# Kernel optimization log

Hardware: AMD Instinct MI355X
Metric: run time of the kernel (lower is better)

Reference implementation:

```python
import jax, jax.numpy as jnp
import numpy as np

N, E, C_IN, C_OUT, NHEADS = 100000, 1600000, 128, 128, 4


def setup_inputs() -> dict:
    key = jax.random.key(0)
    k1, k2, k3, k4 = jax.random.split(key, 4)
    x = jax.random.normal(k1, (N, C_IN), dtype=jnp.float32)
    edge_index = jax.random.randint(k2, (2, E), 0, N, dtype=jnp.int32)
    batch_slices_x = jnp.array([0, N], dtype=jnp.int32)
    # glorot-style init scale
    weight = jax.random.normal(k3, (C_IN, C_OUT), dtype=jnp.float32) * (1.0 / np.sqrt(C_IN))
    att_weight = jax.random.normal(k4, (1, NHEADS, 2 * (C_OUT // NHEADS)), dtype=jnp.float32) * 0.1
    return {"x": x, "edge_index": edge_index, "batch_slices_x": batch_slices_x,
            "weight": weight, "att_weight": att_weight}


def reference(x, edge_index, batch_slices_x, weight, att_weight):
    # Eval-mode VotePoolLayer: hard attention via per-source-node argmax (scatter_max),
    # cat head-combine, no bias, att_act = identity, then graph pruning (relabel=False).
    n = x.shape[0]
    nheads = att_weight.shape[1]
    c1h = att_weight.shape[2] // 2  # out_channels per head

    h = (x @ weight).reshape(n, nheads, c1h)  # (N, H, c)
    w_j = att_weight[0, :, :c1h]              # (H, c) weights for source (x_j)
    w_i = att_weight[0, :, c1h:]              # (H, c) weights for target (x_i)
    # alpha[e,h] = sum_c h[src[e],h,c]*w_j[h,c] + h[dst[e],h,c]*w_i[h,c]
    s_j = jnp.einsum('nhc,hc->nh', h, w_j)    # (N, H)
    s_i = jnp.einsum('nhc,hc->nh', h, w_i)    # (N, H)

    src, dst = edge_index[0], edge_index[1]
    alpha = s_j[src] + s_i[dst]               # (E, H)

    # scatter_max argmax over edges grouped by src, per head -> one-hot alpha
    e = alpha.shape[0]
    seg_max = jax.ops.segment_max(alpha, src, num_segments=n)  # (N, H)
    is_max = alpha == seg_max[src]                             # (E, H)
    eids = jnp.arange(e, dtype=jnp.int32)[:, None]             # (E, 1)
    cand = jnp.where(is_max, eids, jnp.int32(e))
    seg_argmax = jax.ops.segment_min(cand, src, num_segments=n)  # (N, H) edge ids
    alpha_1hot = (eids == seg_argmax[src]).astype(h.dtype)       # (E, H)

    # message passing: weighted source features, scatter-add at destination
    msg = h[src] * alpha_1hot[:, :, None]                        # (E, H, c)
    out = jax.ops.segment_sum(msg, dst, num_segments=n)          # (N, H, c)
    out = out.reshape(n, nheads * c1h)                           # cat combine

    # edge selection (eval branch): alpha.sum(dim=1) > 0
    edge_select = alpha_1hot.sum(axis=1) > 0                     # (E,)

    # prune (relabel=False): nodes = unique(dst[edge_select]); keep edges with both
    # endpoints in node set; zero out features of the selected nodes.
    node_mask = jnp.zeros(n, dtype=jnp.int32).at[dst].max(edge_select.astype(jnp.int32)) > 0
    edge_keep = node_mask[src] & node_mask[dst]                  # (E,) subgraph edge mask
    x_out = jnp.where(node_mask[:, None], jnp.float32(0), out)

    return x_out, edge_keep, node_mask, batch_slices_x
```

## Files before the change

kernel.cpp:

```cpp
#include <hip/hip_runtime.h>
#include <stdint.h>

typedef unsigned long long u64;
typedef unsigned int u32;
typedef unsigned short u16;
typedef u32 u32x4 __attribute__((ext_vector_type(4)));
typedef float f32x4 __attribute__((ext_vector_type(4)));

#define CIN 128
#define NN 100000
#define EE 1600000

__device__ __forceinline__ float bf2f(u16 v) {
    union { u32 u; float f; } cv;
    cv.u = ((u32)v) << 16;
    return cv.f;
}

__device__ __forceinline__ u16 f2bf(float f) {
    u32 b = __float_as_uint(f);
    return (u16)((b + 0x7FFFu + ((b >> 16) & 1u)) >> 16);
}

__device__ __forceinline__ u32 mono32(float f) {
    u32 u = __float_as_uint(f);
    return ((int)u >= 0) ? (u | 0x80000000u) : ~u;
}

__global__ __launch_bounds__(256, 4) void k_s(const u16* __restrict__ x,
                                              const u16* __restrict__ W,
                                              const u16* __restrict__ att,
                                              ushort4* __restrict__ sjb,
                                              ushort4* __restrict__ sib,
                                              u32x4* __restrict__ xout16, int n_xout16,
                                              u32x4* __restrict__ seg16, int n_seg16,
                                              int* __restrict__ nm, int n_nodes) {
    int stride = gridDim.x * blockDim.x;
    int tid = blockIdx.x * blockDim.x + threadIdx.x;
    u32x4 z = { 0, 0, 0, 0 };
    for (int i = tid; i < n_xout16; i += stride) __builtin_nontemporal_store(z, &xout16[i]);
    for (int i = tid; i < n_seg16; i += stride) __builtin_nontemporal_store(z, &seg16[i]);
    for (int i = tid; i < n_nodes; i += stride) nm[i] = 0;

    __shared__ float Vl[1024];
    for (int slot = threadIdx.x; slot < 1024; slot += 256) {
        int k = slot >> 3, h8 = slot & 7;
        int head = h8 & 3;
        int off = (h8 < 4) ? 0 : 32;
        float acc = 0.0f;
        #pragma unroll
        for (int c = 0; c < 32; ++c)
            acc += bf2f(W[k * CIN + head * 32 + c]) * bf2f(att[head * 64 + off + c]);
        Vl[slot] = acc;
    }
    __syncthreads();

    for (int n = tid; n < n_nodes; n += stride) {
        const uint4* row = (const uint4*)(x + (size_t)n * CIN);
        float acc[8];
        #pragma unroll
        for (int h = 0; h < 8; ++h) acc[h] = 0.0f;
        #pragma unroll 4
        for (int q = 0; q < 16; ++q) {
            uint4 v = row[q];
            u32 w[4] = { v.x, v.y, v.z, v.w };
            #pragma unroll
            for (int j = 0; j < 4; ++j) {
                float x0 = bf2f((u16)(w[j] & 0xFFFFu));
                float x1 = bf2f((u16)(w[j] >> 16));
                int k0 = q * 8 + j * 2;
                #pragma unroll
                for (int h = 0; h < 8; ++h) acc[h] += x0 * Vl[k0 * 8 + h];
                #pragma unroll
                for (int h = 0; h < 8; ++h) acc[h] += x1 * Vl[(k0 + 1) * 8 + h];
            }
        }
        ushort4 a, b;
        a.x = f2bf(acc[0]); a.y = f2bf(acc[1]); a.z = f2bf(acc[2]); a.w = f2bf(acc[3]);
        b.x = f2bf(acc[4]); b.y = f2bf(acc[5]); b.z = f2bf(acc[6]); b.w = f2bf(acc[7]);
        sjb[n] = a;
        sib[n] = b;
    }
}

__global__ __launch_bounds__(256) void k_edge(const int* __restrict__ ei,
                                              const ushort4* __restrict__ sjb,
                                              const ushort4* __restrict__ sib,
                                              u64* __restrict__ seg, int n_edges) {
    int e = blockIdx.x * blockDim.x + threadIdx.x;
    if (e >= n_edges) return;
    int src = ei[e], dst = ei[n_edges + e];
    ushort4 sj = sjb[src];
    ushort4 si = sib[dst];
    u64 lo = (u64)(u32)(~(u32)e);
    u64* slot = seg + (size_t)src * 4;
    ulonglong2 c01 = *(const ulonglong2*)(slot);
    ulonglong2 c23 = *(const ulonglong2*)(slot + 2);
    u64 k0 = ((u64)mono32(bf2f(sj.x) + bf2f(si.x)) << 32) | lo;
    u64 k1 = ((u64)mono32(bf2f(sj.y) + bf2f(si.y)) << 32) | lo;
    u64 k2 = ((u64)mono32(bf2f(sj.z) + bf2f(si.z)) << 32) | lo;
    u64 k3 = ((u64)mono32(bf2f(sj.w) + bf2f(si.w)) << 32) | lo;
    if (k0 > c01.x) atomicMax(&slot[0], k0);
    if (k1 > c01.y) atomicMax(&slot[1], k1);
    if (k2 > c23.x) atomicMax(&slot[2], k2);
    if (k3 > c23.y) atomicMax(&slot[3], k3);
}

__global__ void k_select(const int* __restrict__ ei, const u64* __restrict__ seg,
                         int* __restrict__ nm, int n4, int n_edges) {
    int t = blockIdx.x * blockDim.x + threadIdx.x;
    if (t >= n4) return;
    u64 m = seg[t];
    if (m) {
        int e = (int)(~(u32)m);
        nm[ei[n_edges + e]] = 1;
    }
}

__global__ void k_final(const int* __restrict__ ei, const int* __restrict__ nm,
                        const int* __restrict__ slices, float* __restrict__ out,
                        int n_edges, int n_nodes, int ek_off, int nm_off, int sl_off) {
    int t = blockIdx.x * blockDim.x + threadIdx.x;
    int e0 = 4 * t;
    if (e0 < n_edges) {
        int4 srcs = ((const int4*)ei)[t];
        int4 dsts = ((const int4*)(ei + n_edges))[t];
        f32x4 v;
        v.x = (nm[srcs.x] & nm[dsts.x]) ? 1.0f : 0.0f;
        v.y = (nm[srcs.y] & nm[dsts.y]) ? 1.0f : 0.0f;
        v.z = (nm[srcs.z] & nm[dsts.z]) ? 1.0f : 0.0f;
        v.w = (nm[srcs.w] & nm[dsts.w]) ? 1.0f : 0.0f;
        __builtin_nontemporal_store(v, &((f32x4*)(out + ek_off))[t]);
    }
    if (t < n_nodes) out[nm_off + t] = nm[t] ? 1.0f : 0.0f;
    if (t < 2) out[sl_off + t] = (float)slices[t];
}

extern "C" void kernel_launch(void* const* d_in, const int* in_sizes, int n_in,
                              void* d_out, int out_size, void* d_ws, size_t ws_size,
                              hipStream_t stream) {
    const u16* x = nullptr; const int* ei = nullptr; const int* sl = nullptr;
    const u16* W = nullptr; const u16* att = nullptr;
    for (int i = 0; i < n_in; ++i) {
        switch (in_sizes[i]) {
            case NN * CIN:   x   = (const u16*)d_in[i]; break;
            case 2 * EE:     ei  = (const int*)d_in[i]; break;
            case 2:          sl  = (const int*)d_in[i]; break;
            case CIN * CIN:  W   = (const u16*)d_in[i]; break;
            case 256:        att = (const u16*)d_in[i]; break;
            default: break;
        }
    }
    if (!x || !ei || !sl || !W || !att) return;

    float* out = (float*)d_out;
    const int N = NN;
    const int E = EE;
    const int N4 = N * 4;

    const int ek_off = N * CIN;
    const int nm_off = ek_off + E;
    const int sl_off = nm_off + N;

    char* ws = (char*)d_ws;
    ushort4* sjb = (ushort4*)(ws);
    ushort4* sib = (ushort4*)(ws + (size_t)N * 8);
    int*     nm  = (int*)    (ws + (size_t)N * 16);
    u64*     seg = (u64*)    (ws + (size_t)N * 20);

    const int n_xout16 = N * CIN / 4;
    const int n_seg16  = N4 / 2;

    k_s<<<1280, 256, 0, stream>>>(x, W, att, sjb, sib,
                                  (u32x4*)out, n_xout16,
                                  (u32x4*)seg, n_seg16, nm, N);
    k_edge<<<(E + 255) / 256, 256, 0, stream>>>(ei, sjb, sib, seg, E);
    k_select<<<(N4 + 255) / 256, 256, 0, stream>>>(ei, seg, nm, N4, E);
    k_final<<<(E / 4 + 255) / 256, 256, 0, stream>>>(ei, nm, sl, out, E, N, ek_off, nm_off, sl_off);
}
```

Before: 206.7 us.

## Drop source score from per-source argmax and batch four edges per thread

Within a segment grouped by src, s_j[src] is a constant offset, so the per-source argmax depends only on s_i[dst]. The change stops computing and storing s_j. It precomputes s_i as monotone 16-bit bf16 keys and packs them directly into the high bits of the 64-bit atomicMax key. This halves the node-score work and removes one random gather per edge. k_edge now handles four edges per thread with vector nontemporal index loads, and k_final also uses nontemporal index loads. Ties are now decided on bf16 s_i values rather than on the rounded fp32 sum, which could pick a different edge in rare near-tie cases.

```diff
diff --git a/kernel.cpp b/kernel.cpp
--- a/kernel.cpp
+++ b/kernel.cpp
@@ -6,6 +6,7 @@
 typedef unsigned short u16;
 typedef u32 u32x4 __attribute__((ext_vector_type(4)));
 typedef float f32x4 __attribute__((ext_vector_type(4)));
+typedef int i32x4 __attribute__((ext_vector_type(4)));
 
 #define CIN 128
 #define NN 100000
@@ -22,15 +23,13 @@
     return (u16)((b + 0x7FFFu + ((b >> 16) & 1u)) >> 16);
 }
 
-__device__ __forceinline__ u32 mono32(float f) {
-    u32 u = __float_as_uint(f);
-    return ((int)u >= 0) ? (u | 0x80000000u) : ~u;
+__device__ __forceinline__ u16 mono16(u16 b) {
+    return (b & 0x8000u) ? (u16)~b : (u16)(b | 0x8000u);
 }
 
 __global__ __launch_bounds__(256, 4) void k_s(const u16* __restrict__ x,
                                               const u16* __restrict__ W,
                                               const u16* __restrict__ att,
-                                              ushort4* __restrict__ sjb,
                                               ushort4* __restrict__ sib,
                                               u32x4* __restrict__ xout16, int n_xout16,
                                               u32x4* __restrict__ seg16, int n_seg16,
@@ -42,24 +41,22 @@
     for (int i = tid; i < n_seg16; i += stride) __builtin_nontemporal_store(z, &seg16[i]);
     for (int i = tid; i < n_nodes; i += stride) nm[i] = 0;
 
-    __shared__ float Vl[1024];
-    for (int slot = threadIdx.x; slot < 1024; slot += 256) {
-        int k = slot >> 3, h8 = slot & 7;
-        int head = h8 & 3;
-        int off = (h8 < 4) ? 0 : 32;
+    __shared__ float Vl[512];
+    for (int slot = threadIdx.x; slot < 512; slot += 256) {
+        int k = slot >> 2, head = slot & 3;
         float acc = 0.0f;
         #pragma unroll
         for (int c = 0; c < 32; ++c)
-            acc += bf2f(W[k * CIN + head * 32 + c]) * bf2f(att[head * 64 + off + c]);
+            acc += bf2f(W[k * CIN + head * 32 + c]) * bf2f(att[head * 64 + 32 + c]);
         Vl[slot] = acc;
     }
     __syncthreads();
 
     for (int n = tid; n < n_nodes; n += stride) {
         const uint4* row = (const uint4*)(x + (size_t)n * CIN);
-        float acc[8];
+        float acc[4];
         #pragma unroll
-        for (int h = 0; h < 8; ++h) acc[h] = 0.0f;
+        for (int h = 0; h < 4; ++h) acc[h] = 0.0f;
         #pragma unroll 4
         for (int q = 0; q < 16; ++q) {
             uint4 v = row[q];
@@ -70,40 +67,57 @@
                 float x1 = bf2f((u16)(w[j] >> 16));
                 int k0 = q * 8 + j * 2;
                 #pragma unroll
-                for (int h = 0; h < 8; ++h) acc[h] += x0 * Vl[k0 * 8 + h];
+                for (int h = 0; h < 4; ++h) acc[h] += x0 * Vl[k0 * 4 + h];
                 #pragma unroll
-                for (int h = 0; h < 8; ++h) acc[h] += x1 * Vl[(k0 + 1) * 8 + h];
+                for (int h = 0; h < 4; ++h) acc[h] += x1 * Vl[(k0 + 1) * 4 + h];
             }
         }
-        ushort4 a, b;
-        a.x = f2bf(acc[0]); a.y = f2bf(acc[1]); a.z = f2bf(acc[2]); a.w = f2bf(acc[3]);
-        b.x = f2bf(acc[4]); b.y = f2bf(acc[5]); b.z = f2bf(acc[6]); b.w = f2bf(acc[7]);
-        sjb[n] = a;
-        sib[n] = b;
+        ushort4 a;
+        a.x = mono16(f2bf(acc[0])); a.y = mono16(f2bf(acc[1]));
+        a.z = mono16(f2bf(acc[2])); a.w = mono16(f2bf(acc[3]));
+        sib[n] = a;
     }
 }
 
 __global__ __launch_bounds__(256) void k_edge(const int* __restrict__ ei,
-                                              const ushort4* __restrict__ sjb,
                                               const ushort4* __restrict__ sib,
                                               u64* __restrict__ seg, int n_edges) {
-    int e = blockIdx.x * blockDim.x + threadIdx.x;
-    if (e >= n_edges) return;
-    int src = ei[e], dst = ei[n_edges + e];
-    ushort4 sj = sjb[src];
-    ushort4 si = sib[dst];
-    u64 lo = (u64)(u32)(~(u32)e);
-    u64* slot = seg + (size_t)src * 4;
-    ulonglong2 c01 = *(const ulonglong2*)(slot);
-    ulonglong2 c23 = *(const ulonglong2*)(slot + 2);
-    u64 k0 = ((u64)mono32(bf2f(sj.x) + bf2f(si.x)) << 32) | lo;
-    u64 k1 = ((u64)mono32(bf2f(sj.y) + bf2f(si.y)) << 32) | lo;
-    u64 k2 = ((u64)mono32(bf2f(sj.z) + bf2f(si.z)) << 32) | lo;
-    u64 k3 = ((u64)mono32(bf2f(sj.w) + bf2f(si.w)) << 32) | lo;
-    if (k0 > c01.x) atomicMax(&slot[0], k0);
-    if (k1 > c01.y) atomicMax(&slot[1], k1);
-    if (k2 > c23.x) atomicMax(&slot[2], k2);
-    if (k3 > c23.y) atomicMax(&slot[3], k3);
+    int t = blockIdx.x * blockDim.x + threadIdx.x;
+    int e0 = t * 4;
+    if (e0 >= n_edges) return;
+    i32x4 s4 = __builtin_nontemporal_load(((const i32x4*)ei) + t);
+    i32x4 d4 = __builtin_nontemporal_load(((const i32x4*)(ei + n_edges)) + t);
+
+    ushort4 m0 = sib[d4.x];
+    ushort4 m1 = sib[d4.y];
+    ushort4 m2 = sib[d4.z];
+    ushort4 m3 = sib[d4.w];
+
+    u64* r0 = seg + (size_t)s4.x * 4;
+    u64* r1 = seg + (size_t)s4.y * 4;
+    u64* r2 = seg + (size_t)s4.z * 4;
+    u64* r3 = seg + (size_t)s4.w * 4;
+    ulonglong2 a0 = *(const ulonglong2*)(r0), b0 = *(const ulonglong2*)(r0 + 2);
+    ulonglong2 a1 = *(const ulonglong2*)(r1), b1 = *(const ulonglong2*)(r1 + 2);
+    ulonglong2 a2 = *(const ulonglong2*)(r2), b2 = *(const ulonglong2*)(r2 + 2);
+    ulonglong2 a3 = *(const ulonglong2*)(r3), b3 = *(const ulonglong2*)(r3 + 2);
+
+    #define EDGE(i, mi, ai, bi, ri) {                                          \
+        u64 lo = (u64)(u32)~(u32)(e0 + i);                                     \
+        u64 k0 = ((u64)mi.x << 48) | lo;                                       \
+        u64 k1 = ((u64)mi.y << 48) | lo;                                       \
+        u64 k2 = ((u64)mi.z << 48) | lo;                                       \
+        u64 k3 = ((u64)mi.w << 48) | lo;                                       \
+        if (k0 > ai.x) atomicMax(&ri[0], k0);                                  \
+        if (k1 > ai.y) atomicMax(&ri[1], k1);                                  \
+        if (k2 > bi.x) atomicMax(&ri[2], k2);                                  \
+        if (k3 > bi.y) atomicMax(&ri[3], k3);                                  \
+    }
+    EDGE(0, m0, a0, b0, r0)
+    EDGE(1, m1, a1, b1, r1)
+    EDGE(2, m2, a2, b2, r2)
+    EDGE(3, m3, a3, b3, r3)
+    #undef EDGE
 }
 
 __global__ void k_select(const int* __restrict__ ei, const u64* __restrict__ seg,
@@ -123,8 +137,8 @@
     int t = blockIdx.x * blockDim.x + threadIdx.x;
     int e0 = 4 * t;
     if (e0 < n_edges) {
-        int4 srcs = ((const int4*)ei)[t];
-        int4 dsts = ((const int4*)(ei + n_edges))[t];
+        i32x4 srcs = __builtin_nontemporal_load(((const i32x4*)ei) + t);
+        i32x4 dsts = __builtin_nontemporal_load(((const i32x4*)(ei + n_edges)) + t);
         f32x4 v;
         v.x = (nm[srcs.x] & nm[dsts.x]) ? 1.0f : 0.0f;
         v.y = (nm[srcs.y] & nm[dsts.y]) ? 1.0f : 0.0f;
@@ -163,18 +177,17 @@
     const int sl_off = nm_off + N;
 
     char* ws = (char*)d_ws;
-    ushort4* sjb = (ushort4*)(ws);
-    ushort4* sib = (ushort4*)(ws + (size_t)N * 8);
-    int*     nm  = (int*)    (ws + (size_t)N * 16);
-    u64*     seg = (u64*)    (ws + (size_t)N * 20);
+    ushort4* sib = (ushort4*)(ws);
+    int*     nm  = (int*)    (ws + (size_t)N * 8);
+    u64*     seg = (u64*)    (ws + (size_t)N * 12);
 
     const int n_xout16 = N * CIN / 4;
     const int n_seg16  = N4 / 2;
 
-    k_s<<<1280, 256, 0, stream>>>(x, W, att, sjb, sib,
+    k_s<<<1280, 256, 0, stream>>>(x, W, att, sib,
                                   (u32x4*)out, n_xout16,
                                   (u32x4*)seg, n_seg16, nm, N);
-    k_edge<<<(E + 255) / 256, 256, 0, stream>>>(ei, sjb, sib, seg, E);
+    k_edge<<<(E / 4 + 255) / 256, 256, 0, stream>>>(ei, sib, seg, E);
     k_select<<<(N4 + 255) / 256, 256, 0, stream>>>(ei, seg, nm, N4, E);
     k_final<<<(E / 4 + 255) / 256, 256, 0, stream>>>(ei, nm, sl, out, E, N, ek_off, nm_off, sl_off);
 }
```

Result: slower. 219.7 us (+6.3%).
